# Kernel optimization log

Hardware: AMD Instinct MI355X
Metric: run time of the kernel (lower is better)

## Reference

```python
import jax, jax.numpy as jnp
import numpy as np

D_MODEL = 512
N_HEADS = 8
HEAD_DIM = 64
INNER = N_HEADS * HEAD_DIM
PAD = 128  # flash-attention style tile padding used by the custom kernel


def setup_inputs() -> dict:
    key = jax.random.key(0)
    ks = jax.random.split(key, 5)
    B, S = 2, 2048
    scale = 0.02
    return {
        "hidden_states": jax.random.normal(ks[0], (B, S, D_MODEL), dtype=jnp.float32),
        "Wq": jax.random.normal(ks[1], (D_MODEL, INNER), dtype=jnp.float32) * scale,
        "Wk": jax.random.normal(ks[2], (D_MODEL, INNER), dtype=jnp.float32) * scale,
        "Wv": jax.random.normal(ks[3], (D_MODEL, INNER), dtype=jnp.float32) * scale,
        "Wo": jax.random.normal(ks[4], (INNER, D_MODEL), dtype=jnp.float32) * scale,
    }


def _padded_attention(q, k, v):
    """Emulates torch.ops.knl.fwd: pad seq to a multiple of PAD, run
    non-causal scaled dot-product attention masking padded keys, then
    slice back to the original length. q,k,v: [B, S, INNER]."""
    B, S, _ = q.shape
    pad_len = (-S) % PAD
    Sp = S + pad_len
    pad_cfg = ((0, 0), (0, pad_len), (0, 0))
    qp = jnp.pad(q, pad_cfg)
    kp = jnp.pad(k, pad_cfg)
    vp = jnp.pad(v, pad_cfg)
    # [B, H, Sp, hd]
    qh = qp.reshape(B, Sp, N_HEADS, HEAD_DIM).transpose(0, 2, 1, 3)
    kh = kp.reshape(B, Sp, N_HEADS, HEAD_DIM).transpose(0, 2, 1, 3)
    vh = vp.reshape(B, Sp, N_HEADS, HEAD_DIM).transpose(0, 2, 1, 3)
    scale = 1.0 / np.sqrt(HEAD_DIM).astype(np.float32)
    scores = jnp.einsum("bhqd,bhkd->bhqk", qh, kh) * scale  # [B,H,Sp,Sp]
    key_valid = jnp.arange(Sp) < S  # mask out padded keys
    scores = jnp.where(key_valid[None, None, None, :], scores, jnp.float32(-1e30))
    probs = jax.nn.softmax(scores, axis=-1)
    out = jnp.einsum("bhqk,bhkd->bhqd", probs, vh)  # [B,H,Sp,hd]
    out = out.transpose(0, 2, 1, 3).reshape(B, Sp, INNER)
    return out[:, :S, :]


def reference(hidden_states, Wq, Wk, Wv, Wo):
    q = hidden_states @ Wq
    k = hidden_states @ Wk
    v = hidden_states @ Wv
    attn = _padded_attention(q, k, v)
    return attn @ Wo
```

## Files before the change

### kernel.cpp

```cpp
#include <hip/hip_runtime.h>

using bf16 = __bf16;
using bf16x4 = __attribute__((ext_vector_type(4))) __bf16;
using bf16x8 = __attribute__((ext_vector_type(8))) __bf16;
using floatx4 = __attribute__((ext_vector_type(4))) float;
using half4 = __attribute__((ext_vector_type(4))) _Float16;
using half8 = __attribute__((ext_vector_type(8))) _Float16;

#define D_MODEL 512
#define S_LEN 2048
#define HD 64
#define NH 8
#define M_TOT 4096
#define NSPLIT 4
#define KSPAN (S_LEN / NSPLIT)
#define QSCALE 0.18033688f

__device__ __forceinline__ bf16x8 ld8(const bf16* p) {
    return *reinterpret_cast<const bf16x8*>(p);
}
__device__ __forceinline__ void gl_lds16(const bf16* g, bf16* l) {
    __builtin_amdgcn_global_load_lds(
        (const __attribute__((address_space(1))) void*)g,
        (__attribute__((address_space(3))) void*)l, 16, 0, 0);
}

__global__ __launch_bounds__(256) void prep(const float* __restrict__ w0,
                                            const float* __restrict__ w1,
                                            const float* __restrict__ w2,
                                            const float* __restrict__ w3,
                                            const float* __restrict__ X,
                                            bf16* __restrict__ WT,
                                            bf16* __restrict__ Xb) {
    int z = blockIdx.z;
    if (z == 4) {
        int i = (blockIdx.x * 256 + threadIdx.x) * 8;
        float4 a = *reinterpret_cast<const float4*>(X + i);
        float4 b = *reinterpret_cast<const float4*>(X + i + 4);
        bf16x8 o;
        o[0] = (bf16)a.x; o[1] = (bf16)a.y; o[2] = (bf16)a.z; o[3] = (bf16)a.w;
        o[4] = (bf16)b.x; o[5] = (bf16)b.y; o[6] = (bf16)b.z; o[7] = (bf16)b.w;
        *reinterpret_cast<bf16x8*>(Xb + i) = o;
        return;
    }
    if (blockIdx.x >= 256) return;
    __shared__ float t[32][33];
    const float* in = z == 0 ? w0 : z == 1 ? w1 : z == 2 ? w2 : w3;
    bf16* o = WT + (size_t)z * D_MODEL * D_MODEL;
    int x = threadIdx.x & 31;
    int y = threadIdx.x >> 5;
    int k0 = (blockIdx.x & 15) * 32, n0 = (blockIdx.x >> 4) * 32;
    for (int r = y; r < 32; r += 8) t[r][x] = in[(size_t)(k0 + r) * D_MODEL + n0 + x];
    __syncthreads();
    for (int r = y; r < 32; r += 8) o[(size_t)(n0 + r) * D_MODEL + k0 + x] = (bf16)t[x][r];
}

__global__ __launch_bounds__(256) void gemm_qkvf(const bf16* __restrict__ X,
                                                 const bf16* __restrict__ WT,
                                                 bf16* __restrict__ qk,
                                                 bf16* __restrict__ VT) {
    __shared__ __align__(16) bf16 As[64 * 64];
    __shared__ __align__(16) bf16 Bs[64 * 64];
    int lane = threadIdx.x & 63, wave = threadIdx.x >> 6;
    int l15 = lane & 15, quad = lane >> 4;
    int m0 = blockIdx.x * 64;
    int n0 = blockIdx.y * 64;
    int z = n0 >> 9;
    int h = (n0 >> 6) & 7;
    int wm = (wave & 1) * 32, wn = (wave >> 1) * 32;
    float oscale = (z == 0) ? QSCALE : 1.0f;

    int sr = lane >> 3;
    int sc = (lane & 7) ^ sr;
    const bf16* gA = X  + (size_t)(m0 + wave * 16 + sr) * D_MODEL + sc * 8;
    const bf16* gB = WT + (size_t)(n0 + wave * 16 + sr) * D_MODEL + sc * 8;
    bf16* ldsA = &As[(wave * 16) * 64];
    bf16* ldsB = &Bs[(wave * 16) * 64];
    int rx = l15 & 7;

    floatx4 acc[2][2] = {};
    for (int k0 = 0; k0 < D_MODEL; k0 += 64) {
        __syncthreads();
        gl_lds16(gA + k0, ldsA);
        gl_lds16(gA + (size_t)8 * D_MODEL + k0, ldsA + 8 * 64);
        gl_lds16(gB + k0, ldsB);
        gl_lds16(gB + (size_t)8 * D_MODEL + k0, ldsB + 8 * 64);
        __syncthreads();
        bf16x8 af[2][2], bfr[2][2];
        #pragma unroll
        for (int mt = 0; mt < 2; mt++)
            #pragma unroll
            for (int kh = 0; kh < 2; kh++)
                af[mt][kh] = ld8(&As[(wm + mt * 16 + l15) * 64 + (((quad + 4 * kh) ^ rx)) * 8]);
        #pragma unroll
        for (int nt = 0; nt < 2; nt++)
            #pragma unroll
            for (int kh = 0; kh < 2; kh++)
                bfr[nt][kh] = ld8(&Bs[(wn + nt * 16 + l15) * 64 + (((quad + 4 * kh) ^ rx)) * 8]);
        #pragma unroll
        for (int mt = 0; mt < 2; mt++)
            #pragma unroll
            for (int nt = 0; nt < 2; nt++) {
                acc[mt][nt] = __builtin_amdgcn_mfma_f32_16x16x32_bf16(af[mt][0], bfr[nt][0], acc[mt][nt], 0, 0, 0);
                acc[mt][nt] = __builtin_amdgcn_mfma_f32_16x16x32_bf16(af[mt][1], bfr[nt][1], acc[mt][nt], 0, 0, 0);
            }
    }

    if (z < 2) {
        bf16* dst = qk + (size_t)z * M_TOT * HD * NH;
        #pragma unroll
        for (int mt = 0; mt < 2; mt++)
            #pragma unroll
            for (int nt = 0; nt < 2; nt++)
                #pragma unroll
                for (int r = 0; r < 4; r++) {
                    int m = m0 + wm + mt * 16 + quad * 4 + r;
                    int n = wn + nt * 16 + l15;
                    int b = m >> 11, s = m & 2047;
                    dst[((size_t)(b * NH + h) * S_LEN + s) * HD + n] = (bf16)(acc[mt][nt][r] * oscale);
                }
    } else {
        #pragma unroll
        for (int mt = 0; mt < 2; mt++)
            #pragma unroll
            for (int nt = 0; nt < 2; nt++) {
                int m = m0 + wm + mt * 16 + quad * 4;
                int d = wn + nt * 16 + l15;
                int b = m >> 11, s = m & 2047;
                bf16x4 pk;
                pk[0] = (bf16)acc[mt][nt][0]; pk[1] = (bf16)acc[mt][nt][1];
                pk[2] = (bf16)acc[mt][nt][2]; pk[3] = (bf16)acc[mt][nt][3];
                *reinterpret_cast<bf16x4*>(&VT[((size_t)(b * NH + h) * HD + d) * S_LEN + s]) = pk;
            }
    }
}

__global__ __launch_bounds__(256, 8) void attn_split(const bf16* __restrict__ qg,
                                                     const bf16* __restrict__ kg,
                                                     const bf16* __restrict__ vt,
                                                     _Float16* __restrict__ Opart,
                                                     float* __restrict__ lsum) {
    __shared__ __align__(16) bf16 Kl[64 * 64];
    __shared__ __align__(16) bf16 Vl[64 * 64];
    int tid = threadIdx.x;
    int lane = tid & 63, wave = tid >> 6;
    int l15 = lane & 15, quad = lane >> 4;
    int bh = blockIdx.y, split = blockIdx.z;
    int q0 = blockIdx.x * 64;
    const bf16* qb = qg + (size_t)bh * S_LEN * HD;
    const bf16* kb = kg + (size_t)bh * S_LEN * HD + (size_t)split * KSPAN * HD;
    const bf16* vb = vt + (size_t)bh * HD * S_LEN + split * KSPAN;
    int q = q0 + wave * 16 + l15;
    bf16x8 qf0 = ld8(qb + (size_t)q * HD + quad * 8);
    bf16x8 qf1 = ld8(qb + (size_t)q * HD + 32 + quad * 8);
    floatx4 O[4] = {};
    float l_i = 0.f;

    int sr = lane >> 3;
    int sc = (lane & 7) ^ sr;
    const bf16* gK = kb + (size_t)(wave * 16 + sr) * HD + sc * 8;
    const bf16* gV = vb + (size_t)(wave * 16 + sr) * S_LEN + sc * 8;
    bf16* ldsK = &Kl[(wave * 16) * 64];
    bf16* ldsV = &Vl[(wave * 16) * 64];
    int rx = l15 & 7;
    int sa = ((quad & 1) << 5) + l15;
    int sb = sa + 16;
    bool himux = (quad & 2) != 0;

    for (int kt = 0; kt < KSPAN; kt += 64) {
        __syncthreads();
        gl_lds16(gK + (size_t)kt * HD, ldsK);
        gl_lds16(gK + (size_t)(kt + 8) * HD, ldsK + 8 * 64);
        gl_lds16(gV + kt, ldsV);
        gl_lds16(gV + (size_t)8 * S_LEN + kt, ldsV + 8 * 64);
        __syncthreads();

        floatx4 sc4[4];
        #pragma unroll
        for (int nt = 0; nt < 4; nt++) {
            floatx4 z = {};
            bf16x8 a0 = ld8(&Kl[(nt * 16 + l15) * 64 + (quad ^ rx) * 8]);
            bf16x8 a1 = ld8(&Kl[(nt * 16 + l15) * 64 + ((quad + 4) ^ rx) * 8]);
            z = __builtin_amdgcn_mfma_f32_16x16x32_bf16(a0, qf0, z, 0, 0, 0);
            z = __builtin_amdgcn_mfma_f32_16x16x32_bf16(a1, qf1, z, 0, 0, 0);
            sc4[nt] = z;
        }

        int2 pq[4];
        #pragma unroll
        for (int nt = 0; nt < 4; nt++) {
            bf16x4 pk;
            #pragma unroll
            for (int r = 0; r < 4; r++) {
                float p = exp2f(sc4[nt][r]);
                l_i += p;
                pk[r] = (bf16)p;
            }
            pq[nt] = __builtin_bit_cast(int2, pk);
        }

        bf16x8 pb[2];
        #pragma unroll
        for (int h2 = 0; h2 < 2; h2++) {
            int t0 = __shfl(pq[2 * h2].x,     sa, 64);
            int t1 = __shfl(pq[2 * h2].y,     sa, 64);
            int t2 = __shfl(pq[2 * h2 + 1].x, sa, 64);
            int t3 = __shfl(pq[2 * h2 + 1].y, sa, 64);
            int u0 = __shfl(pq[2 * h2].x,     sb, 64);
            int u1 = __shfl(pq[2 * h2].y,     sb, 64);
            int u2 = __shfl(pq[2 * h2 + 1].x, sb, 64);
            int u3 = __shfl(pq[2 * h2 + 1].y, sb, 64);
            int4 v;
            v.x = himux ? t2 : t0;
            v.y = himux ? t3 : t1;
            v.z = himux ? u2 : u0;
            v.w = himux ? u3 : u1;
            pb[h2] = __builtin_bit_cast(bf16x8, v);
        }

        #pragma unroll
        for (int nt = 0; nt < 4; nt++) {
            bf16x8 v0 = ld8(&Vl[(nt * 16 + l15) * 64 + (quad ^ rx) * 8]);
            bf16x8 v1 = ld8(&Vl[(nt * 16 + l15) * 64 + ((quad + 4) ^ rx) * 8]);
            O[nt] = __builtin_amdgcn_mfma_f32_16x16x32_bf16(v0, pb[0], O[nt], 0, 0, 0);
            O[nt] = __builtin_amdgcn_mfma_f32_16x16x32_bf16(v1, pb[1], O[nt], 0, 0, 0);
        }
    }

    l_i += __shfl_xor(l_i, 16, 64);
    l_i += __shfl_xor(l_i, 32, 64);

    size_t obase = (((size_t)(split * 16 + bh)) * S_LEN + q) * HD;
    #pragma unroll
    for (int nt = 0; nt < 4; nt++) {
        half4 hv;
        hv[0] = (_Float16)O[nt][0]; hv[1] = (_Float16)O[nt][1];
        hv[2] = (_Float16)O[nt][2]; hv[3] = (_Float16)O[nt][3];
        *reinterpret_cast<half4*>(&Opart[obase + nt * 16 + quad * 4]) = hv;
    }
    if (quad == 0)
        lsum[((size_t)(split * 16 + bh)) * S_LEN + q] = l_i;
}

__global__ __launch_bounds__(256) void gemm_outm(const _Float16* __restrict__ Opart,
                                                 const float* __restrict__ lsum,
                                                 const bf16* __restrict__ WoT,
                                                 float* __restrict__ out) {
    __shared__ __align__(16) bf16 As[64 * 64];
    __shared__ __align__(16) bf16 Bs[64 * 64];
    __shared__ float invl[64 * 8];
    int tid = threadIdx.x;
    int lane = tid & 63, wave = tid >> 6;
    int l15 = lane & 15, quad = lane >> 4;
    int m0 = blockIdx.x * 64;
    int n0 = blockIdx.y * 64;
    int wm = (wave & 1) * 32, wn = (wave >> 1) * 32;

    for (int i = tid; i < 512; i += 256) {
        int row = i >> 3, h = i & 7;
        int mm = m0 + row;
        int b = mm >> 11, q = mm & 2047;
        float l = 0.f;
        #pragma unroll
        for (int s = 0; s < NSPLIT; s++)
            l += lsum[((size_t)(s * 16 + b * NH + h)) * S_LEN + q];
        invl[i] = 1.f / l;
    }

    int sr = lane >> 3;
    int sc = (lane & 7) ^ sr;
    const bf16* gB = WoT + (size_t)(n0 + wave * 16 + sr) * D_MODEL + sc * 8;
    bf16* ldsA = &As[(wave * 16) * 64];
    bf16* ldsB = &Bs[(wave * 16) * 64];
    int rx = l15 & 7;

    floatx4 acc[2][2] = {};
    for (int k0 = 0; k0 < D_MODEL; k0 += 64) {
        __syncthreads();
        gl_lds16(gB + k0, ldsB);
        gl_lds16(gB + (size_t)8 * D_MODEL + k0, ldsB + 8 * 64);
        int h = k0 >> 6;
        #pragma unroll
        for (int st = 0; st < 2; st++) {
            int row = wave * 16 + sr + st * 8;
            int mm = m0 + row;
            int b = mm >> 11, q = mm & 2047;
            float iv = invl[row * 8 + h];
            float a8[8] = {};
            #pragma unroll
            for (int s = 0; s < NSPLIT; s++) {
                half8 hp = *reinterpret_cast<const half8*>(
                    &Opart[(((size_t)(s * 16 + b * NH + h)) * S_LEN + q) * HD + sc * 8]);
                #pragma unroll
                for (int j = 0; j < 8; j++) a8[j] += (float)hp[j];
            }
            bf16x8 v;
            #pragma unroll
            for (int j = 0; j < 8; j++) v[j] = (bf16)(a8[j] * iv);
            *reinterpret_cast<bf16x8*>(ldsA + st * 512 + lane * 8) = v;
        }
        __syncthreads();
        bf16x8 af[2][2], bfr[2][2];
        #pragma unroll
        for (int mt = 0; mt < 2; mt++)
            #pragma unroll
            for (int kh = 0; kh < 2; kh++)
                af[mt][kh] = ld8(&As[(wm + mt * 16 + l15) * 64 + (((quad + 4 * kh) ^ rx)) * 8]);
        #pragma unroll
        for (int nt = 0; nt < 2; nt++)
            #pragma unroll
            for (int kh = 0; kh < 2; kh++)
                bfr[nt][kh] = ld8(&Bs[(wn + nt * 16 + l15) * 64 + (((quad + 4 * kh) ^ rx)) * 8]);
        #pragma unroll
        for (int mt = 0; mt < 2; mt++)
            #pragma unroll
            for (int nt = 0; nt < 2; nt++) {
                acc[mt][nt] = __builtin_amdgcn_mfma_f32_16x16x32_bf16(af[mt][0], bfr[nt][0], acc[mt][nt], 0, 0, 0);
                acc[mt][nt] = __builtin_amdgcn_mfma_f32_16x16x32_bf16(af[mt][1], bfr[nt][1], acc[mt][nt], 0, 0, 0);
            }
    }

    #pragma unroll
    for (int mt = 0; mt < 2; mt++)
        #pragma unroll
        for (int nt = 0; nt < 2; nt++)
            #pragma unroll
            for (int r = 0; r < 4; r++) {
                int m = m0 + wm + mt * 16 + quad * 4 + r;
                int n = n0 + wn + nt * 16 + l15;
                out[(size_t)m * D_MODEL + n] = acc[mt][nt][r];
            }
}

extern "C" void kernel_launch(void* const* d_in, const int* in_sizes, int n_in,
                              void* d_out, int out_size, void* d_ws, size_t ws_size,
                              hipStream_t stream) {
    const float* X  = (const float*)d_in[0];
    const float* Wq = (const float*)d_in[1];
    const float* Wk = (const float*)d_in[2];
    const float* Wv = (const float*)d_in[3];
    const float* Wo = (const float*)d_in[4];
    float* out = (float*)d_out;
    bf16* ws  = (bf16*)d_ws;

    bf16* Xb  = ws;
    bf16* WT  = Xb + (size_t)M_TOT * D_MODEL;
    bf16* qk  = WT + (size_t)4 * D_MODEL * D_MODEL;
    bf16* VT  = qk + (size_t)2 * M_TOT * D_MODEL;
    _Float16* Opart = (_Float16*)(VT + (size_t)M_TOT * D_MODEL);
    float* lbuf = (float*)(Opart + (size_t)NSPLIT * 16 * S_LEN * HD);

    prep<<<dim3(1024, 1, 5), 256, 0, stream>>>(Wq, Wk, Wv, Wo, X, WT, Xb);
    gemm_qkvf<<<dim3(64, 24), 256, 0, stream>>>(Xb, WT, qk, VT);
    attn_split<<<dim3(32, 16, NSPLIT), 256, 0, stream>>>(qk,
                                                         qk + (size_t)M_TOT * D_MODEL,
                                                         VT, Opart, lbuf);
    gemm_outm<<<dim3(64, 8), 256, 0, stream>>>(Opart, lbuf,
                                               WT + (size_t)3 * D_MODEL * D_MODEL, out);
}
```

Baseline: 131.8 us.

## Process two query sub-tiles per wave in split attention to reuse K/V fragments

Each wave now handles 32 query rows instead of 16, so every K and V fragment read from LDS feeds two MFMA chains. The block covers 128 queries and the grid's x dimension is halved. This halves K/V global-to-LDS traffic and LDS reads per unit of work. In exchange the kernel uses more registers (launch bounds lowered from 8 to 4) and launches fewer blocks (1024), which may reduce latency hiding.

```diff
diff --git a/kernel.cpp b/kernel.cpp
--- a/kernel.cpp
+++ b/kernel.cpp
@@ -135,7 +135,7 @@
     }
 }
 
-__global__ __launch_bounds__(256, 8) void attn_split(const bf16* __restrict__ qg,
+__global__ __launch_bounds__(256, 4) void attn_split(const bf16* __restrict__ qg,
                                                      const bf16* __restrict__ kg,
                                                      const bf16* __restrict__ vt,
                                                      _Float16* __restrict__ Opart,
@@ -146,15 +146,19 @@
     int lane = tid & 63, wave = tid >> 6;
     int l15 = lane & 15, quad = lane >> 4;
     int bh = blockIdx.y, split = blockIdx.z;
-    int q0 = blockIdx.x * 64;
+    int q0 = blockIdx.x * 128;
     const bf16* qb = qg + (size_t)bh * S_LEN * HD;
     const bf16* kb = kg + (size_t)bh * S_LEN * HD + (size_t)split * KSPAN * HD;
     const bf16* vb = vt + (size_t)bh * HD * S_LEN + split * KSPAN;
-    int q = q0 + wave * 16 + l15;
-    bf16x8 qf0 = ld8(qb + (size_t)q * HD + quad * 8);
-    bf16x8 qf1 = ld8(qb + (size_t)q * HD + 32 + quad * 8);
-    floatx4 O[4] = {};
-    float l_i = 0.f;
+    int qA = q0 + wave * 32 + l15;
+    int qB = qA + 16;
+    bf16x8 qf[2][2];
+    qf[0][0] = ld8(qb + (size_t)qA * HD + quad * 8);
+    qf[0][1] = ld8(qb + (size_t)qA * HD + 32 + quad * 8);
+    qf[1][0] = ld8(qb + (size_t)qB * HD + quad * 8);
+    qf[1][1] = ld8(qb + (size_t)qB * HD + 32 + quad * 8);
+    floatx4 O[2][4] = {};
+    float l_i[2] = {0.f, 0.f};
 
     int sr = lane >> 3;
     int sc = (lane & 7) ^ sr;
@@ -175,71 +179,82 @@
         gl_lds16(gV + (size_t)8 * S_LEN + kt, ldsV + 8 * 64);
         __syncthreads();
 
-        floatx4 sc4[4];
+        floatx4 sc4[2][4];
         #pragma unroll
         for (int nt = 0; nt < 4; nt++) {
-            floatx4 z = {};
             bf16x8 a0 = ld8(&Kl[(nt * 16 + l15) * 64 + (quad ^ rx) * 8]);
             bf16x8 a1 = ld8(&Kl[(nt * 16 + l15) * 64 + ((quad + 4) ^ rx) * 8]);
-            z = __builtin_amdgcn_mfma_f32_16x16x32_bf16(a0, qf0, z, 0, 0, 0);
-            z = __builtin_amdgcn_mfma_f32_16x16x32_bf16(a1, qf1, z, 0, 0, 0);
-            sc4[nt] = z;
-        }
-
-        int2 pq[4];
-        #pragma unroll
-        for (int nt = 0; nt < 4; nt++) {
-            bf16x4 pk;
-            #pragma unroll
-            for (int r = 0; r < 4; r++) {
-                float p = exp2f(sc4[nt][r]);
-                l_i += p;
-                pk[r] = (bf16)p;
-            }
-            pq[nt] = __builtin_bit_cast(int2, pk);
-        }
-
-        bf16x8 pb[2];
-        #pragma unroll
-        for (int h2 = 0; h2 < 2; h2++) {
-            int t0 = __shfl(pq[2 * h2].x,     sa, 64);
-            int t1 = __shfl(pq[2 * h2].y,     sa, 64);
-            int t2 = __shfl(pq[2 * h2 + 1].x, sa, 64);
-            int t3 = __shfl(pq[2 * h2 + 1].y, sa, 64);
-            int u0 = __shfl(pq[2 * h2].x,     sb, 64);
-            int u1 = __shfl(pq[2 * h2].y,     sb, 64);
-            int u2 = __shfl(pq[2 * h2 + 1].x, sb, 64);
-            int u3 = __shfl(pq[2 * h2 + 1].y, sb, 64);
-            int4 v;
-            v.x = himux ? t2 : t0;
-            v.y = himux ? t3 : t1;
-            v.z = himux ? u2 : u0;
-            v.w = himux ? u3 : u1;
-            pb[h2] = __builtin_bit_cast(bf16x8, v);
+            #pragma unroll
+            for (int s = 0; s < 2; s++) {
+                floatx4 z = {};
+                z = __builtin_amdgcn_mfma_f32_16x16x32_bf16(a0, qf[s][0], z, 0, 0, 0);
+                z = __builtin_amdgcn_mfma_f32_16x16x32_bf16(a1, qf[s][1], z, 0, 0, 0);
+                sc4[s][nt] = z;
+            }
+        }
+
+        bf16x8 pb[2][2];
+        #pragma unroll
+        for (int s = 0; s < 2; s++) {
+            int2 pq[4];
+            #pragma unroll
+            for (int nt = 0; nt < 4; nt++) {
+                bf16x4 pk;
+                #pragma unroll
+                for (int r = 0; r < 4; r++) {
+                    float p = exp2f(sc4[s][nt][r]);
+                    l_i[s] += p;
+                    pk[r] = (bf16)p;
+                }
+                pq[nt] = __builtin_bit_cast(int2, pk);
+            }
+            #pragma unroll
+            for (int h2 = 0; h2 < 2; h2++) {
+                int t0 = __shfl(pq[2 * h2].x,     sa, 64);
+                int t1 = __shfl(pq[2 * h2].y,     sa, 64);
+                int t2 = __shfl(pq[2 * h2 + 1].x, sa, 64);
+                int t3 = __shfl(pq[2 * h2 + 1].y, sa, 64);
+                int u0 = __shfl(pq[2 * h2].x,     sb, 64);
+                int u1 = __shfl(pq[2 * h2].y,     sb, 64);
+                int u2 = __shfl(pq[2 * h2 + 1].x, sb, 64);
+                int u3 = __shfl(pq[2 * h2 + 1].y, sb, 64);
+                int4 v;
+                v.x = himux ? t2 : t0;
+                v.y = himux ? t3 : t1;
+                v.z = himux ? u2 : u0;
+                v.w = himux ? u3 : u1;
+                pb[s][h2] = __builtin_bit_cast(bf16x8, v);
+            }
         }
 
         #pragma unroll
         for (int nt = 0; nt < 4; nt++) {
             bf16x8 v0 = ld8(&Vl[(nt * 16 + l15) * 64 + (quad ^ rx) * 8]);
             bf16x8 v1 = ld8(&Vl[(nt * 16 + l15) * 64 + ((quad + 4) ^ rx) * 8]);
-            O[nt] = __builtin_amdgcn_mfma_f32_16x16x32_bf16(v0, pb[0], O[nt], 0, 0, 0);
-            O[nt] = __builtin_amdgcn_mfma_f32_16x16x32_bf16(v1, pb[1], O[nt], 0, 0, 0);
-        }
-    }
-
-    l_i += __shfl_xor(l_i, 16, 64);
-    l_i += __shfl_xor(l_i, 32, 64);
-
-    size_t obase = (((size_t)(split * 16 + bh)) * S_LEN + q) * HD;
+            #pragma unroll
+            for (int s = 0; s < 2; s++) {
+                O[s][nt] = __builtin_amdgcn_mfma_f32_16x16x32_bf16(v0, pb[s][0], O[s][nt], 0, 0, 0);
+                O[s][nt] = __builtin_amdgcn_mfma_f32_16x16x32_bf16(v1, pb[s][1], O[s][nt], 0, 0, 0);
+            }
+        }
+    }
+
     #pragma unroll
-    for (int nt = 0; nt < 4; nt++) {
-        half4 hv;
-        hv[0] = (_Float16)O[nt][0]; hv[1] = (_Float16)O[nt][1];
-        hv[2] = (_Float16)O[nt][2]; hv[3] = (_Float16)O[nt][3];
-        *reinterpret_cast<half4*>(&Opart[obase + nt * 16 + quad * 4]) = hv;
-    }
-    if (quad == 0)
-        lsum[((size_t)(split * 16 + bh)) * S_LEN + q] = l_i;
+    for (int s = 0; s < 2; s++) {
+        l_i[s] += __shfl_xor(l_i[s], 16, 64);
+        l_i[s] += __shfl_xor(l_i[s], 32, 64);
+        int q = (s == 0) ? qA : qB;
+        size_t obase = (((size_t)(split * 16 + bh)) * S_LEN + q) * HD;
+        #pragma unroll
+        for (int nt = 0; nt < 4; nt++) {
+            half4 hv;
+            hv[0] = (_Float16)O[s][nt][0]; hv[1] = (_Float16)O[s][nt][1];
+            hv[2] = (_Float16)O[s][nt][2]; hv[3] = (_Float16)O[s][nt][3];
+            *reinterpret_cast<half4*>(&Opart[obase + nt * 16 + quad * 4]) = hv;
+        }
+        if (quad == 0)
+            lsum[((size_t)(split * 16 + bh)) * S_LEN + q] = l_i[s];
+    }
 }
 
 __global__ __launch_bounds__(256) void gemm_outm(const _Float16* __restrict__ Opart,
@@ -352,7 +367,7 @@
 
     prep<<<dim3(1024, 1, 5), 256, 0, stream>>>(Wq, Wk, Wv, Wo, X, WT, Xb);
     gemm_qkvf<<<dim3(64, 24), 256, 0, stream>>>(Xb, WT, qk, VT);
-    attn_split<<<dim3(32, 16, NSPLIT), 256, 0, stream>>>(qk,
+    attn_split<<<dim3(16, 16, NSPLIT), 256, 0, stream>>>(qk,
                                                          qk + (size_t)M_TOT * D_MODEL,
                                                          VT, Opart, lbuf);
     gemm_outm<<<dim3(64, 8), 256, 0, stream>>>(Opart, lbuf,
```

Result: no change. 132.6 us (+0.6%).

## Double-buffer QKV GEMM LDS tiles and load attention K/V directly from global

Applied to the files above, without the earlier changes.

The QKV projection GEMM now double-buffers its A/B LDS tiles, prefetching the next K-slice while computing the current one, with one barrier per iteration instead of two. The split attention kernel drops LDS staging and both barriers, and each wave loads K and V^T fragments directly from global memory (relying on L1/L2 for reuse across the four waves). Its occupancy hint drops from 8 to 4 blocks per CU. This trades barrier and LDS overhead for redundant global and cache traffic in attention. The lower occupancy bound may also reduce latency hiding.

```diff
diff --git a/kernel.cpp b/kernel.cpp
--- a/kernel.cpp
+++ b/kernel.cpp
@@ -59,8 +59,8 @@
                                                  const bf16* __restrict__ WT,
                                                  bf16* __restrict__ qk,
                                                  bf16* __restrict__ VT) {
-    __shared__ __align__(16) bf16 As[64 * 64];
-    __shared__ __align__(16) bf16 Bs[64 * 64];
+    __shared__ __align__(16) bf16 As[2][64 * 64];
+    __shared__ __align__(16) bf16 Bs[2][64 * 64];
     int lane = threadIdx.x & 63, wave = threadIdx.x >> 6;
     int l15 = lane & 15, quad = lane >> 4;
     int m0 = blockIdx.x * 64;
@@ -74,29 +74,35 @@
     int sc = (lane & 7) ^ sr;
     const bf16* gA = X  + (size_t)(m0 + wave * 16 + sr) * D_MODEL + sc * 8;
     const bf16* gB = WT + (size_t)(n0 + wave * 16 + sr) * D_MODEL + sc * 8;
-    bf16* ldsA = &As[(wave * 16) * 64];
-    bf16* ldsB = &Bs[(wave * 16) * 64];
+    int ldsOff = (wave * 16) * 64;
     int rx = l15 & 7;
 
+    gl_lds16(gA, &As[0][ldsOff]);
+    gl_lds16(gA + (size_t)8 * D_MODEL, &As[0][ldsOff + 8 * 64]);
+    gl_lds16(gB, &Bs[0][ldsOff]);
+    gl_lds16(gB + (size_t)8 * D_MODEL, &Bs[0][ldsOff + 8 * 64]);
+    __syncthreads();
+
     floatx4 acc[2][2] = {};
+    int cur = 0;
     for (int k0 = 0; k0 < D_MODEL; k0 += 64) {
-        __syncthreads();
-        gl_lds16(gA + k0, ldsA);
-        gl_lds16(gA + (size_t)8 * D_MODEL + k0, ldsA + 8 * 64);
-        gl_lds16(gB + k0, ldsB);
-        gl_lds16(gB + (size_t)8 * D_MODEL + k0, ldsB + 8 * 64);
-        __syncthreads();
+        if (k0 + 64 < D_MODEL) {
+            gl_lds16(gA + k0 + 64, &As[cur ^ 1][ldsOff]);
+            gl_lds16(gA + (size_t)8 * D_MODEL + k0 + 64, &As[cur ^ 1][ldsOff + 8 * 64]);
+            gl_lds16(gB + k0 + 64, &Bs[cur ^ 1][ldsOff]);
+            gl_lds16(gB + (size_t)8 * D_MODEL + k0 + 64, &Bs[cur ^ 1][ldsOff + 8 * 64]);
+        }
         bf16x8 af[2][2], bfr[2][2];
         #pragma unroll
         for (int mt = 0; mt < 2; mt++)
             #pragma unroll
             for (int kh = 0; kh < 2; kh++)
-                af[mt][kh] = ld8(&As[(wm + mt * 16 + l15) * 64 + (((quad + 4 * kh) ^ rx)) * 8]);
+                af[mt][kh] = ld8(&As[cur][(wm + mt * 16 + l15) * 64 + (((quad + 4 * kh) ^ rx)) * 8]);
         #pragma unroll
         for (int nt = 0; nt < 2; nt++)
             #pragma unroll
             for (int kh = 0; kh < 2; kh++)
-                bfr[nt][kh] = ld8(&Bs[(wn + nt * 16 + l15) * 64 + (((quad + 4 * kh) ^ rx)) * 8]);
+                bfr[nt][kh] = ld8(&Bs[cur][(wn + nt * 16 + l15) * 64 + (((quad + 4 * kh) ^ rx)) * 8]);
         #pragma unroll
         for (int mt = 0; mt < 2; mt++)
             #pragma unroll
@@ -104,6 +110,8 @@
                 acc[mt][nt] = __builtin_amdgcn_mfma_f32_16x16x32_bf16(af[mt][0], bfr[nt][0], acc[mt][nt], 0, 0, 0);
                 acc[mt][nt] = __builtin_amdgcn_mfma_f32_16x16x32_bf16(af[mt][1], bfr[nt][1], acc[mt][nt], 0, 0, 0);
             }
+        __syncthreads();
+        cur ^= 1;
     }
 
     if (z < 2) {
@@ -135,13 +143,11 @@
     }
 }
 
-__global__ __launch_bounds__(256, 8) void attn_split(const bf16* __restrict__ qg,
+__global__ __launch_bounds__(256, 4) void attn_split(const bf16* __restrict__ qg,
                                                      const bf16* __restrict__ kg,
                                                      const bf16* __restrict__ vt,
                                                      _Float16* __restrict__ Opart,
                                                      float* __restrict__ lsum) {
-    __shared__ __align__(16) bf16 Kl[64 * 64];
-    __shared__ __align__(16) bf16 Vl[64 * 64];
     int tid = threadIdx.x;
     int lane = tid & 63, wave = tid >> 6;
     int l15 = lane & 15, quad = lane >> 4;
@@ -156,31 +162,18 @@
     floatx4 O[4] = {};
     float l_i = 0.f;
 
-    int sr = lane >> 3;
-    int sc = (lane & 7) ^ sr;
-    const bf16* gK = kb + (size_t)(wave * 16 + sr) * HD + sc * 8;
-    const bf16* gV = vb + (size_t)(wave * 16 + sr) * S_LEN + sc * 8;
-    bf16* ldsK = &Kl[(wave * 16) * 64];
-    bf16* ldsV = &Vl[(wave * 16) * 64];
-    int rx = l15 & 7;
     int sa = ((quad & 1) << 5) + l15;
     int sb = sa + 16;
     bool himux = (quad & 2) != 0;
 
     for (int kt = 0; kt < KSPAN; kt += 64) {
-        __syncthreads();
-        gl_lds16(gK + (size_t)kt * HD, ldsK);
-        gl_lds16(gK + (size_t)(kt + 8) * HD, ldsK + 8 * 64);
-        gl_lds16(gV + kt, ldsV);
-        gl_lds16(gV + (size_t)8 * S_LEN + kt, ldsV + 8 * 64);
-        __syncthreads();
-
         floatx4 sc4[4];
         #pragma unroll
         for (int nt = 0; nt < 4; nt++) {
+            const bf16* krow = kb + (size_t)(kt + nt * 16 + l15) * HD;
+            bf16x8 a0 = ld8(krow + quad * 8);
+            bf16x8 a1 = ld8(krow + 32 + quad * 8);
             floatx4 z = {};
-            bf16x8 a0 = ld8(&Kl[(nt * 16 + l15) * 64 + (quad ^ rx) * 8]);
-            bf16x8 a1 = ld8(&Kl[(nt * 16 + l15) * 64 + ((quad + 4) ^ rx) * 8]);
             z = __builtin_amdgcn_mfma_f32_16x16x32_bf16(a0, qf0, z, 0, 0, 0);
             z = __builtin_amdgcn_mfma_f32_16x16x32_bf16(a1, qf1, z, 0, 0, 0);
             sc4[nt] = z;
@@ -220,8 +213,9 @@
 
         #pragma unroll
         for (int nt = 0; nt < 4; nt++) {
-            bf16x8 v0 = ld8(&Vl[(nt * 16 + l15) * 64 + (quad ^ rx) * 8]);
-            bf16x8 v1 = ld8(&Vl[(nt * 16 + l15) * 64 + ((quad + 4) ^ rx) * 8]);
+            const bf16* vrow = vb + (size_t)(nt * 16 + l15) * S_LEN + kt;
+            bf16x8 v0 = ld8(vrow + quad * 8);
+            bf16x8 v1 = ld8(vrow + 32 + quad * 8);
             O[nt] = __builtin_amdgcn_mfma_f32_16x16x32_bf16(v0, pb[0], O[nt], 0, 0, 0);
             O[nt] = __builtin_amdgcn_mfma_f32_16x16x32_bf16(v1, pb[1], O[nt], 0, 0, 0);
         }
```

After: 229.1 us. 73.9% more time.
